# Performance work log

Measured on AMD Instinct MI355X. Metric: run time of the kernel, lower is better.

The kernel has to match this reference:

```python
import jax, jax.numpy as jnp
import numpy as np

NB, NG, E1, E2 = 100000, 20000, 400000, 40000
F, FE, H, D = 128, 16, 4, 32
OUT = H * D


def segment_softmax(data, segment_ids, num_segments):
    # data: [E, H, 1]; numerically stable softmax over segments (per head)
    m = jax.ops.segment_max(data, segment_ids, num_segments=num_segments)
    e = jnp.exp(data - m[segment_ids])
    s = jax.ops.segment_sum(e, segment_ids, num_segments=num_segments)
    return e / (s[segment_ids] + 1e-8)


def setup_inputs() -> dict:
    key = jax.random.key(0)
    ks = jax.random.split(key, 16)
    inv = lambda n: 1.0 / np.sqrt(n)
    return {
        'bus_x': jax.random.normal(ks[0], (NB, F), jnp.float32),
        'gen_x': jax.random.normal(ks[1], (NG, F), jnp.float32),
        'ef_line': jax.random.normal(ks[2], (E1, FE), jnp.float32),
        'w_proj_bus': jax.random.normal(ks[3], (F, OUT), jnp.float32) * inv(F),
        'b_proj_bus': jnp.zeros((OUT,), jnp.float32),
        'w_proj_gen': jax.random.normal(ks[4], (F, OUT), jnp.float32) * inv(F),
        'b_proj_gen': jnp.zeros((OUT,), jnp.float32),
        'w_edge_line': jax.random.normal(ks[5], (FE, OUT), jnp.float32) * inv(FE),
        'b_edge_line': jnp.zeros((OUT,), jnp.float32),
        'a_line': jax.random.normal(ks[6], (3 * D,), jnp.float32) * inv(3 * D),
        'a_feeds': jax.random.normal(ks[7], (3 * D,), jnp.float32) * inv(3 * D),
        'w_upd_bus': jax.random.normal(ks[8], (2 * OUT, OUT), jnp.float32) * inv(2 * OUT),
        'b_upd_bus': jnp.zeros((OUT,), jnp.float32),
        'w_upd_gen': jax.random.normal(ks[9], (2 * OUT, OUT), jnp.float32) * inv(2 * OUT),
        'b_upd_gen': jnp.zeros((OUT,), jnp.float32),
        'senders_line': jax.random.randint(ks[10], (E1,), 0, NB, jnp.int32),
        'receivers_line': jax.random.randint(ks[11], (E1,), 0, NB, jnp.int32),
        'senders_feeds': jax.random.randint(ks[12], (E2,), 0, NB, jnp.int32),
        'receivers_feeds': jax.random.randint(ks[13], (E2,), 0, NG, jnp.int32),
    }


def _edge_attn_aggregate(p_src_nodes, p_dst_nodes, senders, receivers, attn_w,
                         edge_proj, num_dst):
    # gather per-edge features: [E, H, D]
    src = p_src_nodes[senders]
    dst = p_dst_nodes[receivers]
    concat = jnp.concatenate([src, dst, src + edge_proj], axis=-1)  # [E, H, 3D]
    score = jnp.einsum('ehd,d->eh', concat, attn_w)[..., None]      # [E, H, 1]
    score = jax.nn.leaky_relu(score, negative_slope=0.2)
    alpha = segment_softmax(score, receivers, num_dst)              # [E, H, 1]
    msgs = src * alpha                                              # [E, H, D]
    return jax.ops.segment_sum(msgs, receivers, num_segments=num_dst)


def reference(bus_x, gen_x, ef_line, w_proj_bus, b_proj_bus, w_proj_gen, b_proj_gen,
              w_edge_line, b_edge_line, a_line, a_feeds, w_upd_bus, b_upd_bus,
              w_upd_gen, b_upd_gen, senders_line, receivers_line, senders_feeds,
              receivers_feeds):
    # node projections -> [N, H, D]
    p_bus = (bus_x @ w_proj_bus + b_proj_bus).reshape(NB, H, D)
    p_gen = (gen_x @ w_proj_gen + b_proj_gen).reshape(NG, H, D)

    # edge type ('bus','line','bus') with edge features
    e_proj = (ef_line @ w_edge_line + b_edge_line).reshape(E1, H, D)
    new_bus = _edge_attn_aggregate(p_bus, p_bus, senders_line, receivers_line,
                                   a_line, e_proj, NB)

    # edge type ('bus','feeds','gen') without edge features (edge_feats_proj = 0)
    new_gen = _edge_attn_aggregate(p_bus, p_gen, senders_feeds, receivers_feeds,
                                   a_feeds, 0.0, NG)

    # per-node-type update MLP on [proj || aggregated] flattened to 2*OUT
    bus_in = jnp.concatenate([p_bus, new_bus], axis=-1).reshape(NB, 2 * OUT)
    gen_in = jnp.concatenate([p_gen, new_gen], axis=-1).reshape(NG, 2 * OUT)
    bus_out = jax.nn.relu(bus_in @ w_upd_bus + b_upd_bus)
    gen_out = jax.nn.relu(gen_in @ w_upd_gen + b_upd_gen)
    # concat node types along axis 0 for a single output array [NB+NG, OUT]
    return jnp.concatenate([bus_out, gen_out], axis=0)
```

## Files before the change

kernel.cpp:

```cpp
#include <hip/hip_runtime.h>
#include <hip/hip_bf16.h>

#define NBUS 100000
#define NGEN 20000
#define NE1  400000
#define NE2  40000

#define CAP_L 24
#define CAP_F 16

#define OFF_PB    0
#define OFF_PG    6400000
#define OFF_AGL   7680000
#define OFF_AGF   14080000
#define OFF_SSL   15360000
#define OFF_SDL   15760000
#define OFF_SSF   16160000
#define OFF_SDF   16560000
#define OFF_CNTL  16640000
#define OFF_CNTF  16740000
#define OFF_RECL  16760000
#define OFF_RECF  35960000
#define OFF_WTPB  38520000
#define OFF_WTPG  38528192
#define OFF_WTUB  38536384
#define OFF_WTUG  38552768
#define OFF_COEF  38569152
#define OFF_VLINE 38569280
#define CNT_TOTAL (NBUS + NGEN)

typedef short short8 __attribute__((ext_vector_type(8)));
typedef float f32x4 __attribute__((ext_vector_type(4)));

__device__ __forceinline__ unsigned short f2bf(float f) {
  unsigned u = __float_as_uint(f);
  return (unsigned short)((u + 0x7fffu + ((u >> 16) & 1u)) >> 16);
}
__device__ __forceinline__ float bf2f(unsigned v) {
  return __uint_as_float(v << 16);
}

__device__ __forceinline__ f32x4 mfma16(short8 a, short8 b, f32x4 c) {
  return __builtin_amdgcn_mfma_f32_16x16x32_bf16(a, b, c, 0, 0, 0);
}

__global__ void prep_kernel(const float* __restrict__ a_line, const float* __restrict__ a_feeds,
                            const float* __restrict__ w_edge, const float* __restrict__ b_edge,
                            float* __restrict__ coefs, float* __restrict__ vline) {
  int t = threadIdx.x;
  if (t < 32) {
    coefs[t]      = a_line[t] + a_line[64 + t];
    coefs[32 + t] = a_line[32 + t];
    coefs[64 + t] = a_feeds[t] + a_feeds[64 + t];
    coefs[96 + t] = a_feeds[32 + t];
  }
  if (t < 64) {
    int h = t >> 4, f = t & 15;
    float s = 0.f;
    for (int d = 0; d < 32; ++d) s += w_edge[f * 128 + h * 32 + d] * a_line[64 + d];
    vline[h * 16 + f] = s;
  }
  if (t < 4) {
    float s = 0.f;
    for (int d = 0; d < 32; ++d) s += b_edge[t * 32 + d] * a_line[64 + d];
    vline[64 + t] = s;
  }
}

__global__ __launch_bounds__(256) void transpose_all(
    const float* __restrict__ s0, const float* __restrict__ s1,
    const float* __restrict__ s2, const float* __restrict__ s3,
    unsigned short* __restrict__ d0, unsigned short* __restrict__ d1,
    unsigned short* __restrict__ d2, unsigned short* __restrict__ d3,
    int* __restrict__ cnt_all) {
  int fb = (blockIdx.z * gridDim.y + blockIdx.y) * gridDim.x + blockIdx.x;
  int gid = fb * 256 + threadIdx.x;
  for (int i = gid; i < CNT_TOTAL; i += 128 * 256) cnt_all[i] = 0;
  int z = blockIdx.z;
  const float* src = z == 0 ? s0 : (z == 1 ? s1 : (z == 2 ? s2 : s3));
  unsigned short* dst = z == 0 ? d0 : (z == 1 ? d1 : (z == 2 ? d2 : d3));
  const int K = z < 2 ? 128 : 256;
  const int N = 128;
  __shared__ float t[32][33];
  int n0 = blockIdx.x * 32, k0 = blockIdx.y * 32;
  if (k0 >= K) return;
  int tx = threadIdx.x & 31, ty = threadIdx.x >> 5;
#pragma unroll
  for (int i = 0; i < 4; ++i) {
    int k = k0 + ty + i * 8, n = n0 + tx;
    t[ty + i * 8][tx] = src[(size_t)k * N + n];
  }
  __syncthreads();
#pragma unroll
  for (int i = 0; i < 4; ++i) {
    int n = n0 + ty + i * 8, k = k0 + tx;
    dst[(size_t)n * K + k] = f2bf(t[tx][ty + i * 8]);
  }
}

#define NS_BUS (NBUS * 4)
__global__ __launch_bounds__(256) void node_scores2(
    const unsigned short* __restrict__ PB, const unsigned short* __restrict__ PG,
    const float* __restrict__ coefs,
    float* __restrict__ ssl, float* __restrict__ sdl,
    float* __restrict__ ssf, float* __restrict__ sdf) {
  __shared__ float cs[128];
  int tid = threadIdx.x;
  if (tid < 128) cs[tid] = coefs[tid];
  __syncthreads();
  int gid = blockIdx.x * 256 + tid;
  if (gid < NS_BUS) {
    int r = gid >> 2, h = gid & 3;
    const unsigned short* base = PB + (size_t)r * 128 + h * 32;
    float a0 = 0.f, a1 = 0.f, a2 = 0.f;
#pragma unroll
    for (int j = 0; j < 4; ++j) {
      uint4 u = *(const uint4*)(base + j * 8);
      float x[8] = {bf2f(u.x & 0xffffu), bf2f(u.x >> 16), bf2f(u.y & 0xffffu), bf2f(u.y >> 16),
                    bf2f(u.z & 0xffffu), bf2f(u.z >> 16), bf2f(u.w & 0xffffu), bf2f(u.w >> 16)};
#pragma unroll
      for (int t = 0; t < 8; ++t) {
        a0 += x[t] * cs[j * 8 + t];
        a1 += x[t] * cs[32 + j * 8 + t];
        a2 += x[t] * cs[64 + j * 8 + t];
      }
    }
    ssl[gid] = a0; sdl[gid] = a1; ssf[gid] = a2;
  } else {
    int gid2 = gid - NS_BUS;
    if (gid2 < NGEN * 4) {
      int r = gid2 >> 2, h = gid2 & 3;
      const unsigned short* base = PG + (size_t)r * 128 + h * 32;
      float a3 = 0.f;
#pragma unroll
      for (int j = 0; j < 4; ++j) {
        uint4 u = *(const uint4*)(base + j * 8);
        float x[8] = {bf2f(u.x & 0xffffu), bf2f(u.x >> 16), bf2f(u.y & 0xffffu), bf2f(u.y >> 16),
                      bf2f(u.z & 0xffffu), bf2f(u.z >> 16), bf2f(u.w & 0xffffu), bf2f(u.w >> 16)};
#pragma unroll
        for (int t = 0; t < 8; ++t) a3 += x[t] * cs[96 + j * 8 + t];
      }
      sdf[gid2] = a3;
    }
  }
}

#define E1_BLOCKS ((NE1 + 255) / 256)
__global__ __launch_bounds__(256) void edge_scores2(
    const int* __restrict__ snd_l, const int* __restrict__ rcv_l,
    const float* __restrict__ ef, const float* __restrict__ ssl,
    const float* __restrict__ sdl, const float* __restrict__ vline,
    float* __restrict__ rec_l, int* __restrict__ cnt_l,
    const int* __restrict__ snd_f, const int* __restrict__ rcv_f,
    const float* __restrict__ ssf, const float* __restrict__ sdf,
    float* __restrict__ rec_f, int* __restrict__ cnt_f) {
  bool isline = blockIdx.x < E1_BLOCKS;
  __shared__ float vs[68];
  int tid = threadIdx.x;
  if (isline && tid < 68) vs[tid] = vline[tid];
  __syncthreads();
  const int* snd  = isline ? snd_l : snd_f;
  const int* rcv  = isline ? rcv_l : rcv_f;
  const float* ss = isline ? ssl : ssf;
  const float* sds = isline ? sdl : sdf;
  float* rec      = isline ? rec_l : rec_f;
  int* cnt        = isline ? cnt_l : cnt_f;
  const int cap   = isline ? CAP_L : CAP_F;
  const int E     = isline ? NE1 : NE2;
  int e = (isline ? blockIdx.x : blockIdx.x - E1_BLOCKS) * 256 + tid;
  if (e >= E) return;
  int s = snd[e], r = rcv[e];
  float4 sa = *(const float4*)(ss + (size_t)s * 4);
  float4 sb = *(const float4*)(sds + (size_t)r * 4);
  float se[4] = {0.f, 0.f, 0.f, 0.f};
  if (isline) {
    float f[16];
#pragma unroll
    for (int j = 0; j < 4; ++j) *(float4*)&f[j * 4] = *(const float4*)(ef + (size_t)e * 16 + j * 4);
#pragma unroll
    for (int h = 0; h < 4; ++h) {
      float acc = vs[64 + h];
#pragma unroll
      for (int j = 0; j < 16; ++j) acc += f[j] * vs[h * 16 + j];
      se[h] = acc;
    }
  }
  float sc[4] = {sa.x + sb.x + se[0], sa.y + sb.y + se[1],
                 sa.z + sb.z + se[2], sa.w + sb.w + se[3]};
#pragma unroll
  for (int h = 0; h < 4; ++h) {
    float v = sc[h];
    v = v > 0.f ? v : 0.2f * v;
    sc[h] = __expf(v);
  }
  int slot = atomicAdd(cnt + r, 1);
  if (slot < cap) {
    float* p = rec + ((size_t)r * cap + slot) * 8;
    *(float4*)p = make_float4(sc[0], sc[1], sc[2], sc[3]);
    ((int*)p)[4] = s;
  }
}

#define GL_BLOCKS ((NBUS + 3) / 4)
__global__ __launch_bounds__(256) void gather2(
    const int* __restrict__ cnt_l, const float* __restrict__ rec_l,
    unsigned short* __restrict__ agg_l,
    const int* __restrict__ cnt_f, const float* __restrict__ rec_f,
    unsigned short* __restrict__ agg_f,
    const unsigned short* __restrict__ P) {
  bool isline = blockIdx.x < GL_BLOCKS;
  int wv = threadIdx.x >> 6;
  int r = (isline ? blockIdx.x : blockIdx.x - GL_BLOCKS) * 4 + wv;
  r = __builtin_amdgcn_readfirstlane(r);
  const int* cnt = isline ? cnt_l : cnt_f;
  const float* rec = isline ? rec_l : rec_f;
  unsigned short* agg = isline ? agg_l : agg_f;
  const int cap = isline ? CAP_L : CAP_F;
  const int R = isline ? NBUS : NGEN;
  if (r >= R) return;
  const int lane = threadIdx.x & 63;
  const int h = lane >> 4;
  int deg = cnt[r];
  deg = deg < cap ? deg : cap;
  deg = __builtin_amdgcn_readfirstlane(deg);
  const float* rb = rec + (size_t)r * cap * 8;
  const float* sp = rb + h;
  const unsigned short* Pl = P + lane * 2;

  float ex[8]; int sd[8];
#pragma unroll
  for (int i = 0; i < 8; ++i) {
    if (i < deg) {
      ex[i] = sp[i * 8];
      sd[i] = ((const int*)rb)[i * 8 + 4];
    } else { ex[i] = 0.f; sd[i] = 0; }
  }
  float den = 1e-8f;
#pragma unroll
  for (int i = 0; i < 8; ++i) den += ex[i];
  if (deg > 8) {
    for (int i = 8; i < deg; ++i) den += sp[i * 8];
  }
  float dinv = 1.0f / den;
  unsigned pv[8];
#pragma unroll
  for (int i = 0; i < 8; ++i) {
    if (i < deg) {
      int si = __builtin_amdgcn_readfirstlane(sd[i]);
      pv[i] = *(const unsigned*)(Pl + (size_t)si * 128);
    }
  }
  float a0 = 0.f, a1 = 0.f;
#pragma unroll
  for (int i = 0; i < 8; ++i) {
    if (i < deg) {
      float wi = ex[i] * dinv;
      a0 += bf2f(pv[i] & 0xffffu) * wi;
      a1 += bf2f(pv[i] >> 16) * wi;
    }
  }
  if (deg > 8) {
    for (int i = 8; i < deg; ++i) {
      float wi = sp[i * 8] * dinv;
      int si = __builtin_amdgcn_readfirstlane(((const int*)rb)[i * 8 + 4]);
      unsigned pvt = *(const unsigned*)(Pl + (size_t)si * 128);
      a0 += bf2f(pvt & 0xffffu) * wi;
      a1 += bf2f(pvt >> 16) * wi;
    }
  }
  unsigned pk = (unsigned)f2bf(a0) | ((unsigned)f2bf(a1) << 16);
  *(unsigned*)(agg + (size_t)r * 128 + lane * 2) = pk;
}

#define MBLK 128
template <bool UPDATE>
__global__ __launch_bounds__(256, 2) void mfma_gemm2(
    const float* __restrict__ XFb, const float* __restrict__ XFg,
    const unsigned short* __restrict__ PBb, const unsigned short* __restrict__ AGb,
    const unsigned short* __restrict__ PBg, const unsigned short* __restrict__ AGg,
    const unsigned short* __restrict__ WTb, const unsigned short* __restrict__ WTg,
    const float* __restrict__ Bb, const float* __restrict__ Bg,
    float* __restrict__ YFb, float* __restrict__ YFg,
    unsigned short* __restrict__ YBb, unsigned short* __restrict__ YBg,
    int Mb, int Mg, int nbb) {
  __shared__ unsigned short xs[MBLK * 128];
  __shared__ unsigned short ws[128 * 128];
  const bool isb = (int)blockIdx.x < nbb;
  const float* XF = isb ? XFb : XFg;
  const unsigned short* PB = isb ? PBb : PBg;
  const unsigned short* AG = isb ? AGb : AGg;
  const unsigned short* WT = isb ? WTb : WTg;
  const float* B = isb ? Bb : Bg;
  float* YF = isb ? YFb : YFg;
  unsigned short* YB = isb ? YBb : YBg;
  const int M = isb ? Mb : Mg;
  const int bid = isb ? blockIdx.x : blockIdx.x - nbb;
  const int tid = threadIdx.x;
  const int wave = tid >> 6, lane = tid & 63;
  const int l15 = lane & 15, l4 = lane >> 4;
  const int row0 = bid * MBLK;
  const int KCH = UPDATE ? 2 : 1;
  f32x4 acc[2][8] = {};
  for (int kc = 0; kc < KCH; ++kc) {
#pragma unroll
    for (int i = 0; i < 8; ++i) {
      int c = tid + i * 256;
      int r = c >> 4, k16 = c & 15;
      int row = row0 + r;
      uint4 v = make_uint4(0u, 0u, 0u, 0u);
      if (row < M) {
        if (!UPDATE) {
          const float* s = XF + (size_t)row * 128 + k16 * 8;
          float4 f0 = *(const float4*)s;
          float4 f1 = *(const float4*)(s + 4);
          v.x = (unsigned)f2bf(f0.x) | ((unsigned)f2bf(f0.y) << 16);
          v.y = (unsigned)f2bf(f0.z) | ((unsigned)f2bf(f0.w) << 16);
          v.z = (unsigned)f2bf(f1.x) | ((unsigned)f2bf(f1.y) << 16);
          v.w = (unsigned)f2bf(f1.z) | ((unsigned)f2bf(f1.w) << 16);
        } else {
          int kg = kc * 128 + k16 * 8;
          int h = kg >> 6, j = kg & 63;
          const unsigned short* s = (j < 32)
              ? PB + (size_t)row * 128 + h * 32 + j
              : AG + (size_t)row * 128 + h * 32 + (j - 32);
          v = *(const uint4*)s;
        }
      }
      int byte = r * 256 + ((k16 * 16) ^ ((r & 7) << 4));
      *(uint4*)((char*)xs + byte) = v;
    }
#pragma unroll
    for (int i = 0; i < 8; ++i) {
      int c = tid + i * 256;
      int col = c >> 4, k16 = c & 15;
      uint4 v = *(const uint4*)(WT + (size_t)col * (KCH * 128) + kc * 128 + k16 * 8);
      int byte = col * 256 + ((k16 * 16) ^ ((col & 7) << 4));
      *(uint4*)((char*)ws + byte) = v;
    }
    __syncthreads();
    const int wrow = wave * 32;
    const int sw = (l15 & 7) << 4;
#pragma unroll
    for (int ks = 0; ks < 4; ++ks) {
      int kb = (ks * 64 + l4 * 16) ^ sw;
      short8 a0 = *(const short8*)((const char*)xs + (wrow + l15) * 256 + kb);
      short8 a1 = *(const short8*)((const char*)xs + (wrow + 16 + l15) * 256 + kb);
#pragma unroll
      for (int ni = 0; ni < 8; ++ni) {
        short8 b = *(const short8*)((const char*)ws + (ni * 16 + l15) * 256 + kb);
        acc[0][ni] = mfma16(a0, b, acc[0][ni]);
        acc[1][ni] = mfma16(a1, b, acc[1][ni]);
      }
    }
    __syncthreads();
  }
  float bb[8];
#pragma unroll
  for (int ni = 0; ni < 8; ++ni) bb[ni] = B[ni * 16 + l15];
  const int rbase = row0 + wave * 32 + l4 * 4;
#pragma unroll
  for (int mi = 0; mi < 2; ++mi) {
#pragma unroll
    for (int reg = 0; reg < 4; ++reg) {
      int row = rbase + mi * 16 + reg;
      if (row < M) {
#pragma unroll
        for (int ni = 0; ni < 8; ++ni) {
          float v = acc[mi][ni][reg] + bb[ni];
          if (UPDATE) {
            YF[(size_t)row * 128 + ni * 16 + l15] = fmaxf(v, 0.f);
          } else {
            YB[(size_t)row * 128 + ni * 16 + l15] = f2bf(v);
          }
        }
      }
    }
  }
}

extern "C" void kernel_launch(void* const* d_in, const int* in_sizes, int n_in,
                              void* d_out, int out_size, void* d_ws, size_t ws_size,
                              hipStream_t stream) {
  const float* bus_x       = (const float*)d_in[0];
  const float* gen_x       = (const float*)d_in[1];
  const float* ef_line     = (const float*)d_in[2];
  const float* w_proj_bus  = (const float*)d_in[3];
  const float* b_proj_bus  = (const float*)d_in[4];
  const float* w_proj_gen  = (const float*)d_in[5];
  const float* b_proj_gen  = (const float*)d_in[6];
  const float* w_edge_line = (const float*)d_in[7];
  const float* b_edge_line = (const float*)d_in[8];
  const float* a_line      = (const float*)d_in[9];
  const float* a_feeds     = (const float*)d_in[10];
  const float* w_upd_bus   = (const float*)d_in[11];
  const float* b_upd_bus   = (const float*)d_in[12];
  const float* w_upd_gen   = (const float*)d_in[13];
  const float* b_upd_gen   = (const float*)d_in[14];
  const int* senders_line    = (const int*)d_in[15];
  const int* receivers_line  = (const int*)d_in[16];
  const int* senders_feeds   = (const int*)d_in[17];
  const int* receivers_feeds = (const int*)d_in[18];
  float* out = (float*)d_out;
  float* ws  = (float*)d_ws;

  unsigned short* p_bus  = (unsigned short*)(ws + OFF_PB);
  unsigned short* p_gen  = (unsigned short*)(ws + OFF_PG);
  unsigned short* agg_l  = (unsigned short*)(ws + OFF_AGL);
  unsigned short* agg_f  = (unsigned short*)(ws + OFF_AGF);
  float* ssl    = ws + OFF_SSL;
  float* sdl    = ws + OFF_SDL;
  float* ssf    = ws + OFF_SSF;
  float* sdf    = ws + OFF_SDF;
  int*   cnt_l  = (int*)(ws + OFF_CNTL);
  int*   cnt_f  = (int*)(ws + OFF_CNTF);
  float* rec_l  = ws + OFF_RECL;
  float* rec_f  = ws + OFF_RECF;
  unsigned short* wt_pb = (unsigned short*)(ws + OFF_WTPB);
  unsigned short* wt_pg = (unsigned short*)(ws + OFF_WTPG);
  unsigned short* wt_ub = (unsigned short*)(ws + OFF_WTUB);
  unsigned short* wt_ug = (unsigned short*)(ws + OFF_WTUG);
  float* coefs  = ws + OFF_COEF;
  float* vline  = ws + OFF_VLINE;

  prep_kernel<<<1, 128, 0, stream>>>(a_line, a_feeds, w_edge_line, b_edge_line, coefs, vline);

  transpose_all<<<dim3(4, 8, 4), 256, 0, stream>>>(w_proj_bus, w_proj_gen, w_upd_bus, w_upd_gen,
                                                   wt_pb, wt_pg, wt_ub, wt_ug, cnt_l);

  const int NBB = (NBUS + MBLK - 1) / MBLK;
  const int NGB = (NGEN + MBLK - 1) / MBLK;

  mfma_gemm2<false><<<NBB + NGB, 256, 0, stream>>>(
      bus_x, gen_x, nullptr, nullptr, nullptr, nullptr, wt_pb, wt_pg,
      b_proj_bus, b_proj_gen, nullptr, nullptr, p_bus, p_gen, NBUS, NGEN, NBB);

  node_scores2<<<((NBUS + NGEN) * 4 + 255) / 256, 256, 0, stream>>>(
      p_bus, p_gen, coefs, ssl, sdl, ssf, sdf);

  edge_scores2<<<E1_BLOCKS + (NE2 + 255) / 256, 256, 0, stream>>>(
      senders_line, receivers_line, ef_line, ssl, sdl, vline, rec_l, cnt_l,
      senders_feeds, receivers_feeds, ssf, sdf, rec_f, cnt_f);

  gather2<<<GL_BLOCKS + (NGEN + 3) / 4, 256, 0, stream>>>(
      cnt_l, rec_l, agg_l, cnt_f, rec_f, agg_f, p_bus);

  mfma_gemm2<true><<<NBB + NGB, 256, 0, stream>>>(
      nullptr, nullptr, p_bus, agg_l, p_gen, agg_f, wt_ub, wt_ug,
      b_upd_bus, b_upd_gen, out, out + (size_t)NBUS * 128, nullptr, nullptr,
      NBUS, NGEN, NBB);
}
```

Before: 131.0 us.

## Split edge records into per-head score and sender arrays; fold prep into transpose

Replaces the interleaved 8-float per-edge record with a structure-of-arrays layout: scores stored per receiver per head contiguously and sender indices in a separate array. The gather kernel can then load the first eight scores and senders with vector float4/int4 loads instead of strided scalar loads, and the record buffers shrink. It also folds the single-block prep kernel into an otherwise idle block of the transpose kernel, removing one launch. The edge kernel now issues five scattered scalar stores per edge instead of a vector store plus a scalar store, and the gather reads the first eight slots unconditionally even when the degree is lower.

```diff
diff --git a/kernel.cpp b/kernel.cpp
--- a/kernel.cpp
+++ b/kernel.cpp
@@ -19,14 +19,16 @@
 #define OFF_SDF   16560000
 #define OFF_CNTL  16640000
 #define OFF_CNTF  16740000
-#define OFF_RECL  16760000
-#define OFF_RECF  35960000
-#define OFF_WTPB  38520000
-#define OFF_WTPG  38528192
-#define OFF_WTUB  38536384
-#define OFF_WTUG  38552768
-#define OFF_COEF  38569152
-#define OFF_VLINE 38569280
+#define OFF_SCL   16760000
+#define OFF_SNL   26360000
+#define OFF_SCF   28760000
+#define OFF_SNF   30040000
+#define OFF_WTPB  30360000
+#define OFF_WTPG  30368192
+#define OFF_WTUB  30376384
+#define OFF_WTUG  30392768
+#define OFF_COEF  30409152
+#define OFF_VLINE 30409280
 #define CNT_TOTAL (NBUS + NGEN)
 
 typedef short short8 __attribute__((ext_vector_type(8)));
@@ -42,29 +44,6 @@
 
 __device__ __forceinline__ f32x4 mfma16(short8 a, short8 b, f32x4 c) {
   return __builtin_amdgcn_mfma_f32_16x16x32_bf16(a, b, c, 0, 0, 0);
-}
-
-__global__ void prep_kernel(const float* __restrict__ a_line, const float* __restrict__ a_feeds,
-                            const float* __restrict__ w_edge, const float* __restrict__ b_edge,
-                            float* __restrict__ coefs, float* __restrict__ vline) {
-  int t = threadIdx.x;
-  if (t < 32) {
-    coefs[t]      = a_line[t] + a_line[64 + t];
-    coefs[32 + t] = a_line[32 + t];
-    coefs[64 + t] = a_feeds[t] + a_feeds[64 + t];
-    coefs[96 + t] = a_feeds[32 + t];
-  }
-  if (t < 64) {
-    int h = t >> 4, f = t & 15;
-    float s = 0.f;
-    for (int d = 0; d < 32; ++d) s += w_edge[f * 128 + h * 32 + d] * a_line[64 + d];
-    vline[h * 16 + f] = s;
-  }
-  if (t < 4) {
-    float s = 0.f;
-    for (int d = 0; d < 32; ++d) s += b_edge[t * 32 + d] * a_line[64 + d];
-    vline[64 + t] = s;
-  }
 }
 
 __global__ __launch_bounds__(256) void transpose_all(
@@ -72,10 +51,34 @@
     const float* __restrict__ s2, const float* __restrict__ s3,
     unsigned short* __restrict__ d0, unsigned short* __restrict__ d1,
     unsigned short* __restrict__ d2, unsigned short* __restrict__ d3,
-    int* __restrict__ cnt_all) {
+    int* __restrict__ cnt_all,
+    const float* __restrict__ a_line, const float* __restrict__ a_feeds,
+    const float* __restrict__ w_edge, const float* __restrict__ b_edge,
+    float* __restrict__ coefs, float* __restrict__ vline) {
   int fb = (blockIdx.z * gridDim.y + blockIdx.y) * gridDim.x + blockIdx.x;
   int gid = fb * 256 + threadIdx.x;
   for (int i = gid; i < CNT_TOTAL; i += 128 * 256) cnt_all[i] = 0;
+  if (blockIdx.z == 0 && blockIdx.y == 4 && blockIdx.x == 0) {
+    int t = threadIdx.x;
+    if (t < 32) {
+      coefs[t]      = a_line[t] + a_line[64 + t];
+      coefs[32 + t] = a_line[32 + t];
+      coefs[64 + t] = a_feeds[t] + a_feeds[64 + t];
+      coefs[96 + t] = a_feeds[32 + t];
+    }
+    if (t < 64) {
+      int h = t >> 4, f = t & 15;
+      float s = 0.f;
+      for (int d = 0; d < 32; ++d) s += w_edge[f * 128 + h * 32 + d] * a_line[64 + d];
+      vline[h * 16 + f] = s;
+    }
+    if (t < 4) {
+      float s = 0.f;
+      for (int d = 0; d < 32; ++d) s += b_edge[t * 32 + d] * a_line[64 + d];
+      vline[64 + t] = s;
+    }
+    return;
+  }
   int z = blockIdx.z;
   const float* src = z == 0 ? s0 : (z == 1 ? s1 : (z == 2 ? s2 : s3));
   unsigned short* dst = z == 0 ? d0 : (z == 1 ? d1 : (z == 2 ? d2 : d3));
@@ -150,10 +153,10 @@
     const int* __restrict__ snd_l, const int* __restrict__ rcv_l,
     const float* __restrict__ ef, const float* __restrict__ ssl,
     const float* __restrict__ sdl, const float* __restrict__ vline,
-    float* __restrict__ rec_l, int* __restrict__ cnt_l,
+    float* __restrict__ scr_l, int* __restrict__ sna_l, int* __restrict__ cnt_l,
     const int* __restrict__ snd_f, const int* __restrict__ rcv_f,
     const float* __restrict__ ssf, const float* __restrict__ sdf,
-    float* __restrict__ rec_f, int* __restrict__ cnt_f) {
+    float* __restrict__ scr_f, int* __restrict__ sna_f, int* __restrict__ cnt_f) {
   bool isline = blockIdx.x < E1_BLOCKS;
   __shared__ float vs[68];
   int tid = threadIdx.x;
@@ -163,7 +166,8 @@
   const int* rcv  = isline ? rcv_l : rcv_f;
   const float* ss = isline ? ssl : ssf;
   const float* sds = isline ? sdl : sdf;
-  float* rec      = isline ? rec_l : rec_f;
+  float* scr      = isline ? scr_l : scr_f;
+  int* sna        = isline ? sna_l : sna_f;
   int* cnt        = isline ? cnt_l : cnt_f;
   const int cap   = isline ? CAP_L : CAP_F;
   const int E     = isline ? NE1 : NE2;
@@ -195,25 +199,29 @@
   }
   int slot = atomicAdd(cnt + r, 1);
   if (slot < cap) {
-    float* p = rec + ((size_t)r * cap + slot) * 8;
-    *(float4*)p = make_float4(sc[0], sc[1], sc[2], sc[3]);
-    ((int*)p)[4] = s;
+    float* sp = scr + (size_t)r * 4 * cap + slot;
+    sp[0]       = sc[0];
+    sp[cap]     = sc[1];
+    sp[2 * cap] = sc[2];
+    sp[3 * cap] = sc[3];
+    sna[(size_t)r * cap + slot] = s;
   }
 }
 
 #define GL_BLOCKS ((NBUS + 3) / 4)
 __global__ __launch_bounds__(256) void gather2(
-    const int* __restrict__ cnt_l, const float* __restrict__ rec_l,
-    unsigned short* __restrict__ agg_l,
-    const int* __restrict__ cnt_f, const float* __restrict__ rec_f,
-    unsigned short* __restrict__ agg_f,
+    const int* __restrict__ cnt_l, const float* __restrict__ scr_l,
+    const int* __restrict__ sna_l, unsigned short* __restrict__ agg_l,
+    const int* __restrict__ cnt_f, const float* __restrict__ scr_f,
+    const int* __restrict__ sna_f, unsigned short* __restrict__ agg_f,
     const unsigned short* __restrict__ P) {
   bool isline = blockIdx.x < GL_BLOCKS;
   int wv = threadIdx.x >> 6;
   int r = (isline ? blockIdx.x : blockIdx.x - GL_BLOCKS) * 4 + wv;
   r = __builtin_amdgcn_readfirstlane(r);
   const int* cnt = isline ? cnt_l : cnt_f;
-  const float* rec = isline ? rec_l : rec_f;
+  const float* scr = isline ? scr_l : scr_f;
+  const int* sna = isline ? sna_l : sna_f;
   unsigned short* agg = isline ? agg_l : agg_f;
   const int cap = isline ? CAP_L : CAP_F;
   const int R = isline ? NBUS : NGEN;
@@ -223,23 +231,24 @@
   int deg = cnt[r];
   deg = deg < cap ? deg : cap;
   deg = __builtin_amdgcn_readfirstlane(deg);
-  const float* rb = rec + (size_t)r * cap * 8;
-  const float* sp = rb + h;
+  const float* sp = scr + ((size_t)r * 4 + h) * cap;
+  const int* sb = sna + (size_t)r * cap;
   const unsigned short* Pl = P + lane * 2;
 
-  float ex[8]; int sd[8];
-#pragma unroll
-  for (int i = 0; i < 8; ++i) {
-    if (i < deg) {
-      ex[i] = sp[i * 8];
-      sd[i] = ((const int*)rb)[i * 8 + 4];
-    } else { ex[i] = 0.f; sd[i] = 0; }
-  }
+  float4 e0 = *(const float4*)sp;
+  float4 e1 = *(const float4*)(sp + 4);
+  int4 d0 = *(const int4*)sb;
+  int4 d1 = *(const int4*)(sb + 4);
+  float ex[8] = {e0.x, e0.y, e0.z, e0.w, e1.x, e1.y, e1.z, e1.w};
+  int   sd[8] = {d0.x, d0.y, d0.z, d0.w, d1.x, d1.y, d1.z, d1.w};
+#pragma unroll
+  for (int i = 0; i < 8; ++i)
+    if (i >= deg) ex[i] = 0.f;
   float den = 1e-8f;
 #pragma unroll
   for (int i = 0; i < 8; ++i) den += ex[i];
   if (deg > 8) {
-    for (int i = 8; i < deg; ++i) den += sp[i * 8];
+    for (int i = 8; i < deg; ++i) den += sp[i];
   }
   float dinv = 1.0f / den;
   unsigned pv[8];
@@ -261,8 +270,8 @@
   }
   if (deg > 8) {
     for (int i = 8; i < deg; ++i) {
-      float wi = sp[i * 8] * dinv;
-      int si = __builtin_amdgcn_readfirstlane(((const int*)rb)[i * 8 + 4]);
+      float wi = sp[i] * dinv;
+      int si = __builtin_amdgcn_readfirstlane(sb[i]);
       unsigned pvt = *(const unsigned*)(Pl + (size_t)si * 128);
       a0 += bf2f(pvt & 0xffffu) * wi;
       a1 += bf2f(pvt >> 16) * wi;
@@ -413,8 +422,10 @@
   float* sdf    = ws + OFF_SDF;
   int*   cnt_l  = (int*)(ws + OFF_CNTL);
   int*   cnt_f  = (int*)(ws + OFF_CNTF);
-  float* rec_l  = ws + OFF_RECL;
-  float* rec_f  = ws + OFF_RECF;
+  float* scr_l  = ws + OFF_SCL;
+  int*   sna_l  = (int*)(ws + OFF_SNL);
+  float* scr_f  = ws + OFF_SCF;
+  int*   sna_f  = (int*)(ws + OFF_SNF);
   unsigned short* wt_pb = (unsigned short*)(ws + OFF_WTPB);
   unsigned short* wt_pg = (unsigned short*)(ws + OFF_WTPG);
   unsigned short* wt_ub = (unsigned short*)(ws + OFF_WTUB);
@@ -422,10 +433,10 @@
   float* coefs  = ws + OFF_COEF;
   float* vline  = ws + OFF_VLINE;
 
-  prep_kernel<<<1, 128, 0, stream>>>(a_line, a_feeds, w_edge_line, b_edge_line, coefs, vline);
-
-  transpose_all<<<dim3(4, 8, 4), 256, 0, stream>>>(w_proj_bus, w_proj_gen, w_upd_bus, w_upd_gen,
-                                                   wt_pb, wt_pg, wt_ub, wt_ug, cnt_l);
+  transpose_all<<<dim3(4, 8, 4), 256, 0, stream>>>(
+      w_proj_bus, w_proj_gen, w_upd_bus, w_upd_gen,
+      wt_pb, wt_pg, wt_ub, wt_ug, cnt_l,
+      a_line, a_feeds, w_edge_line, b_edge_line, coefs, vline);
 
   const int NBB = (NBUS + MBLK - 1) / MBLK;
   const int NGB = (NGEN + MBLK - 1) / MBLK;
@@ -438,11 +449,11 @@
       p_bus, p_gen, coefs, ssl, sdl, ssf, sdf);
 
   edge_scores2<<<E1_BLOCKS + (NE2 + 255) / 256, 256, 0, stream>>>(
-      senders_line, receivers_line, ef_line, ssl, sdl, vline, rec_l, cnt_l,
-      senders_feeds, receivers_feeds, ssf, sdf, rec_f, cnt_f);
+      senders_line, receivers_line, ef_line, ssl, sdl, vline, scr_l, sna_l, cnt_l,
+      senders_feeds, receivers_feeds, ssf, sdf, scr_f, sna_f, cnt_f);
 
   gather2<<<GL_BLOCKS + (NGEN + 3) / 4, 256, 0, stream>>>(
-      cnt_l, rec_l, agg_l, cnt_f, rec_f, agg_f, p_bus);
+      cnt_l, scr_l, sna_l, agg_l, cnt_f, scr_f, sna_f, agg_f, p_bus);
 
   mfma_gemm2<true><<<NBB + NGB, 256, 0, stream>>>(
       nullptr, nullptr, p_bus, agg_l, p_gen, agg_f, wt_ub, wt_ug,
```

New measurement: 148.6 us. +13.5%, slower.
